# Optimization experiments

Hardware: AMD Instinct MI355X
Metric: run time of the kernel (lower is better)

## Reference

```python
import jax, jax.numpy as jnp
import numpy as np

OUT, IN = 4096, 4096      # weight_shape
VDIM = 8                  # codebook vector_dim
CODEBOOK_SIZE = 256
LEVEL = 2                 # haar_decomposition_level
INV_SQRT2 = 0.7071067811865476


def unpack_bool(packed, shape):
    # packed: int array of bytes (values 0..255); unpack 8 bits per byte (LSB first)
    bits = (packed[:, None] >> jnp.arange(8, dtype=packed.dtype)) & 1  # [n_bytes, 8]
    return bits.reshape(shape)


def inverse_haar(c, level):
    # c: [..., n] orthonormal Haar coefficients laid out [a_L, d_L, d_{L-1}, ..., d_1]
    n = c.shape[-1]
    m = n >> level
    a = c[..., :m]
    while m < n:
        d = c[..., m:2 * m]
        even = (a + d) * INV_SQRT2
        odd = (a - d) * INV_SQRT2
        a = jnp.stack([even, odd], axis=-1).reshape(c.shape[:-1] + (2 * m,))
        m *= 2
    return a


def setup_inputs() -> dict:
    key = jax.random.key(0)
    k1, k2, k3, k4, k5 = jax.random.split(key, 5)
    x = jax.random.normal(k1, (4, 2048, IN), dtype=jnp.float32)
    codebook = jax.random.normal(k2, (CODEBOOK_SIZE, VDIM), dtype=jnp.float32)
    scales = jax.random.uniform(k5, (OUT, 1), dtype=jnp.float32)
    indices = jax.random.randint(k3, (OUT * IN // VDIM,), 0, CODEBOOK_SIZE, dtype=jnp.int32)
    signs_packed = jax.random.randint(k4, (OUT * IN // 8,), 0, 256, dtype=jnp.int32)
    return {"x": x, "codebook": codebook, "scales": scales,
            "indices": indices, "signs_packed": signs_packed}


def reference(x, codebook, scales, indices, signs_packed):
    # codebook gather -> haar-domain magnitudes, reshaped to signs_shape = weight shape
    haar_freq = codebook[indices].reshape(OUT, IN)
    # unpack sign bits and map {0,1} -> {-1,+1}
    signs = 2.0 * unpack_bool(signs_packed, (OUT, IN)).astype(haar_freq.dtype) - 1.0
    haar_freq = haar_freq * signs
    # multi-level inverse Haar wavelet along in_features
    w = inverse_haar(haar_freq, LEVEL)
    w = w * scales  # per-output-row scales
    return jnp.einsum('bsi,oi->bso', x, w)
```

## Files before the change

### kernel.cpp

```cpp
#include <hip/hip_runtime.h>
#include <hip/hip_bf16.h>

typedef unsigned short u16;
typedef unsigned int u32;
typedef float f32x4 __attribute__((ext_vector_type(4)));
typedef u16 u16x4 __attribute__((ext_vector_type(4)));
typedef u16 u16x8 __attribute__((ext_vector_type(8)));
typedef __bf16 bf16x8 __attribute__((ext_vector_type(8)));

#define OUT_DIM 4096
#define IN_DIM  4096
#define M_DIM   8192

__device__ __forceinline__ u16 f2bf(float f) {
  u32 u = __builtin_bit_cast(u32, f);
  return (u16)((u + 0x7FFFu + ((u >> 16) & 1u)) >> 16);
}

__global__ __launch_bounds__(256) void build_w_kernel(
    const float* __restrict__ codebook, const float* __restrict__ scales,
    const int* __restrict__ indices, const int* __restrict__ signs,
    u16* __restrict__ W) {
  __shared__ float c[IN_DIM];
  const int o   = blockIdx.x;
  const int tid = threadIdx.x;
  for (int g = tid; g < IN_DIM / 8; g += 256) {
    const int idx = indices[o * (IN_DIM / 8) + g];
    const int sp  = signs[o * (IN_DIM / 8) + g];
    f32x4 c0 = *(const f32x4*)&codebook[idx * 8];
    f32x4 c1 = *(const f32x4*)&codebook[idx * 8 + 4];
    float v[8] = {c0[0], c0[1], c0[2], c0[3], c1[0], c1[1], c1[2], c1[3]};
#pragma unroll
    for (int j = 0; j < 8; ++j)
      c[g * 8 + j] = ((sp >> j) & 1) ? v[j] : -v[j];
  }
  __syncthreads();
  const float scale = scales[o];
  const float S = 0.70710678118654752440f;
  for (int t = tid; t < IN_DIM / 4; t += 256) {
    float a   = c[t];
    float d1  = c[IN_DIM / 4 + t];
    float d2a = c[IN_DIM / 2 + 2 * t];
    float d2b = c[IN_DIM / 2 + 2 * t + 1];
    float e  = (a + d1) * S;
    float od = (a - d1) * S;
    u16x4 w;
    w[0] = f2bf((e  + d2a) * S * scale);
    w[1] = f2bf((e  - d2a) * S * scale);
    w[2] = f2bf((od + d2b) * S * scale);
    w[3] = f2bf((od - d2b) * S * scale);
    *(u16x4*)&W[(size_t)o * IN_DIM + 4 * t] = w;
  }
}

__global__ __launch_bounds__(256) void cvt_x_kernel(
    const float* __restrict__ X, u16* __restrict__ Xb) {
  const int stride = gridDim.x * blockDim.x;
  const int n8 = (M_DIM * IN_DIM) / 8;
  for (int i = blockIdx.x * blockDim.x + threadIdx.x; i < n8; i += stride) {
    f32x4 a = *(const f32x4*)&X[(size_t)i * 8];
    f32x4 b = *(const f32x4*)&X[(size_t)i * 8 + 4];
    u16x8 r;
    r[0] = f2bf(a[0]); r[1] = f2bf(a[1]); r[2] = f2bf(a[2]); r[3] = f2bf(a[3]);
    r[4] = f2bf(b[0]); r[5] = f2bf(b[1]); r[6] = f2bf(b[2]); r[7] = f2bf(b[3]);
    *(u16x8*)&Xb[(size_t)i * 8] = r;
  }
}

__global__ __launch_bounds__(512, 1) void gemm_bt_kernel(
    const u16* __restrict__ A,
    const u16* __restrict__ B,
    float*     __restrict__ C) {
  constexpr int K   = IN_DIM;
  constexpr int NT  = K / 64;
  constexpr int NIT = NT / 2;
  extern __shared__ char smem[];

  const int tid  = threadIdx.x;
  const int wave = tid >> 6;
  const int lane = tid & 63;

  const int swz = (blockIdx.x & 7) * 64 + (blockIdx.x >> 3);
  const int bm = (swz >> 4) * 256;
  const int bn = (swz & 15) * 256;

  const int wr  = (wave >> 2) * 128;
  const int wc  = (wave & 3) * 64;
  const int fr  = lane & 15;
  const int fkB = (lane >> 4) * 16;

  int offA[2][4], offB[4];
#pragma unroll
  for (int mq = 0; mq < 2; ++mq)
#pragma unroll
    for (int m = 0; m < 4; ++m) {
      int o = (wr + mq * 64 + m * 16 + fr) * 64 + fkB;
      offA[mq][m] = o ^ ((o >> 3) & 0x30);
    }
#pragma unroll
  for (int n = 0; n < 4; ++n) {
    int o = (wc + n * 16 + fr) * 64 + fkB;
    offB[n] = 16384 + (o ^ ((o >> 3) & 0x30));
  }

  const int d0 = tid * 16,        d1 = 8192 + tid * 16;
  const int l0 = d0 ^ ((d0 >> 3) & 0x30), l1 = d1 ^ ((d1 >> 3) & 0x30);
  const u16* srcA0 = A + (size_t)(bm + (d0 >> 6)) * K + ((l0 & 63) >> 1);
  const u16* srcA1 = A + (size_t)(bm + (d1 >> 6)) * K + ((l1 & 63) >> 1);
  const u16* srcB0 = B + (size_t)(bn + (d0 >> 6)) * K + ((l0 & 63) >> 1);
  const u16* srcB1 = B + (size_t)(bn + (d1 >> 6)) * K + ((l1 & 63) >> 1);
  const int ldsW = wave * 1024;

#define GLD(SRC, DST)                                              \
  __builtin_amdgcn_global_load_lds(                                \
      (const __attribute__((address_space(1))) void*)(SRC),        \
      (__attribute__((address_space(3))) void*)(DST), 16, 0, 0)

  auto stageRegion = [&](int bufi, int ks, int tile) {
    char* base = smem + bufi * 65536 + ks * 32768 + ldsW;
    const u16* a0 = srcA0 + tile * 64 + ks * 32;
    const u16* a1 = srcA1 + tile * 64 + ks * 32;
    const u16* b0 = srcB0 + tile * 64 + ks * 32;
    const u16* b1 = srcB1 + tile * 64 + ks * 32;
    GLD(a0, base);
    GLD(a1, base + 8192);
    GLD(b0, base + 16384);
    GLD(b1, base + 24576);
  };

  f32x4 acc[8][4] = {};
  bf16x8 aq[4], bq[4];

  stageRegion(0, 0, 0);
  stageRegion(0, 1, 0);
  stageRegion(1, 0, 1);
  asm volatile("s_waitcnt vmcnt(8)" ::: "memory");
  __builtin_amdgcn_s_barrier();

#define PHASE(BUFI, KS, MQ, READB, STAGE, GATE)                              \
  {                                                                          \
    const char* rb = smem + (BUFI) * 65536 + (KS) * 32768;                   \
    if (READB) {                                                             \
      _Pragma("unroll")                                                      \
      for (int n = 0; n < 4; ++n) bq[n] = *(const bf16x8*)(rb + offB[n]);    \
    }                                                                        \
    _Pragma("unroll")                                                        \
    for (int m = 0; m < 4; ++m) aq[m] = *(const bf16x8*)(rb + offA[MQ][m]);  \
    STAGE;                                                                   \
    GATE;                                                                    \
    __builtin_amdgcn_s_barrier();                                            \
    asm volatile("s_waitcnt lgkmcnt(0)" ::: "memory");                       \
    __builtin_amdgcn_s_setprio(1);                                           \
    _Pragma("unroll")                                                        \
    for (int m = 0; m < 4; ++m)                                              \
      _Pragma("unroll")                                                      \
      for (int n = 0; n < 4; ++n)                                            \
        acc[(MQ) * 4 + m][n] = __builtin_amdgcn_mfma_f32_16x16x32_bf16(      \
            aq[m], bq[n], acc[(MQ) * 4 + m][n], 0, 0, 0);                    \
    __builtin_amdgcn_s_setprio(0);                                           \
  }

#define VM8 asm volatile("s_waitcnt vmcnt(8)" ::: "memory")
#define VM4 asm volatile("s_waitcnt vmcnt(4)" ::: "memory")
#define VM0 asm volatile("s_waitcnt vmcnt(0)" ::: "memory")

  for (int i = 0; i < NIT - 1; ++i) {
    const int t0 = 2 * i;
    PHASE(0, 0, 0, 1, , )
    PHASE(0, 0, 1, 0, stageRegion(1, 1, t0 + 1), VM8)
    PHASE(0, 1, 0, 1, , )
    PHASE(0, 1, 1, 0, stageRegion(0, 0, t0 + 2), VM8)
    PHASE(1, 0, 0, 1, , )
    PHASE(1, 0, 1, 0, stageRegion(0, 1, t0 + 2), VM8)
    PHASE(1, 1, 0, 1, , )
    PHASE(1, 1, 1, 0, stageRegion(1, 0, t0 + 3), VM8)
  }

  PHASE(0, 0, 0, 1, , )
  PHASE(0, 0, 1, 0, stageRegion(1, 1, NT - 1), VM8)
  PHASE(0, 1, 0, 1, , )
  PHASE(0, 1, 1, 0, , VM4)
  PHASE(1, 0, 0, 1, , )
  PHASE(1, 0, 1, 0, , VM0)
  PHASE(1, 1, 0, 1, , )
  PHASE(1, 1, 1, 0, , )
#undef PHASE
#undef GLD
#undef VM8
#undef VM4
#undef VM0

#pragma unroll
  for (int h = 0; h < 8; ++h)
#pragma unroll
    for (int n = 0; n < 4; ++n) {
      const int col = bn + wc + n * 16 + fr;
#pragma unroll
      for (int j = 0; j < 4; ++j) {
        const int row = bm + wr + h * 16 + (lane >> 4) * 4 + j;
        C[(size_t)row * OUT_DIM + col] = acc[h][n][j];
      }
    }
}

extern "C" void kernel_launch(void* const* d_in, const int* in_sizes, int n_in,
                              void* d_out, int out_size, void* d_ws, size_t ws_size,
                              hipStream_t stream) {
  const float* x        = (const float*)d_in[0];
  const float* codebook = (const float*)d_in[1];
  const float* scales   = (const float*)d_in[2];
  const int*   indices  = (const int*)d_in[3];
  const int*   signs    = (const int*)d_in[4];
  float* out = (float*)d_out;

  u16* W  = (u16*)d_ws;
  u16* Xb = (u16*)d_ws + (size_t)OUT_DIM * IN_DIM;

  (void)hipFuncSetAttribute((const void*)gemm_bt_kernel,
                            hipFuncAttributeMaxDynamicSharedMemorySize, 131072);

  build_w_kernel<<<OUT_DIM, 256, 0, stream>>>(codebook, scales, indices, signs, W);
  cvt_x_kernel<<<2048, 256, 0, stream>>>(x, Xb);
  gemm_bt_kernel<<<(M_DIM / 256) * (OUT_DIM / 256), 512, 131072, stream>>>(Xb, W, out);
}
```

Baseline: 277.4 us.

## Restructure GEMM main loop into paired phases with one barrier per k-slice

The GEMM inner loop now handles both 64-row A halves of each k-slice in one PAIR block. It uses a single workgroup barrier per slice instead of two. The second A-half LDS reads are issued after the first batch of MFMAs, so they overlap compute instead of sitting behind a barrier and an explicit lgkmcnt(0). The global-to-LDS prefetch schedule is reworked to stage one region ahead with vmcnt(4) gates. This shortens the prefetch distance from the earlier three-region lead, which risks exposing more global load latency in exchange for less synchronisation.

```diff
diff --git a/kernel.cpp b/kernel.cpp
--- a/kernel.cpp
+++ b/kernel.cpp
@@ -73,7 +73,7 @@
     float*     __restrict__ C) {
   constexpr int K   = IN_DIM;
   constexpr int NT  = K / 64;
-  constexpr int NIT = NT / 2;
+  constexpr int NJ  = NT / 2;
   extern __shared__ char smem[];
 
   const int tid  = threadIdx.x;
@@ -129,66 +129,64 @@
   };
 
   f32x4 acc[8][4] = {};
-  bf16x8 aq[4], bq[4];
-
-  stageRegion(0, 0, 0);
-  stageRegion(0, 1, 0);
-  stageRegion(1, 0, 1);
-  asm volatile("s_waitcnt vmcnt(8)" ::: "memory");
-  __builtin_amdgcn_s_barrier();
-
-#define PHASE(BUFI, KS, MQ, READB, STAGE, GATE)                              \
+  bf16x8 aqA[4], aqB[4], bq[4];
+
+#define VM4 asm volatile("s_waitcnt vmcnt(4)" ::: "memory")
+#define VM0 asm volatile("s_waitcnt vmcnt(0)" ::: "memory")
+#define BARM asm volatile("s_barrier" ::: "memory")
+
+#define PAIR(BUFI, KS, STG, GATE)                                            \
   {                                                                          \
     const char* rb = smem + (BUFI) * 65536 + (KS) * 32768;                   \
-    if (READB) {                                                             \
-      _Pragma("unroll")                                                      \
-      for (int n = 0; n < 4; ++n) bq[n] = *(const bf16x8*)(rb + offB[n]);    \
-    }                                                                        \
-    _Pragma("unroll")                                                        \
-    for (int m = 0; m < 4; ++m) aq[m] = *(const bf16x8*)(rb + offA[MQ][m]);  \
-    STAGE;                                                                   \
+    _Pragma("unroll")                                                        \
+    for (int n = 0; n < 4; ++n) bq[n] = *(const bf16x8*)(rb + offB[n]);      \
+    _Pragma("unroll")                                                        \
+    for (int m = 0; m < 4; ++m) aqA[m] = *(const bf16x8*)(rb + offA[0][m]);  \
+    STG;                                                                     \
     GATE;                                                                    \
-    __builtin_amdgcn_s_barrier();                                            \
-    asm volatile("s_waitcnt lgkmcnt(0)" ::: "memory");                       \
+    BARM;                                                                    \
     __builtin_amdgcn_s_setprio(1);                                           \
     _Pragma("unroll")                                                        \
     for (int m = 0; m < 4; ++m)                                              \
       _Pragma("unroll")                                                      \
       for (int n = 0; n < 4; ++n)                                            \
-        acc[(MQ) * 4 + m][n] = __builtin_amdgcn_mfma_f32_16x16x32_bf16(      \
-            aq[m], bq[n], acc[(MQ) * 4 + m][n], 0, 0, 0);                    \
+        acc[m][n] = __builtin_amdgcn_mfma_f32_16x16x32_bf16(                 \
+            aqA[m], bq[n], acc[m][n], 0, 0, 0);                              \
     __builtin_amdgcn_s_setprio(0);                                           \
-  }
-
-#define VM8 asm volatile("s_waitcnt vmcnt(8)" ::: "memory")
-#define VM4 asm volatile("s_waitcnt vmcnt(4)" ::: "memory")
-#define VM0 asm volatile("s_waitcnt vmcnt(0)" ::: "memory")
-
-  for (int i = 0; i < NIT - 1; ++i) {
-    const int t0 = 2 * i;
-    PHASE(0, 0, 0, 1, , )
-    PHASE(0, 0, 1, 0, stageRegion(1, 1, t0 + 1), VM8)
-    PHASE(0, 1, 0, 1, , )
-    PHASE(0, 1, 1, 0, stageRegion(0, 0, t0 + 2), VM8)
-    PHASE(1, 0, 0, 1, , )
-    PHASE(1, 0, 1, 0, stageRegion(0, 1, t0 + 2), VM8)
-    PHASE(1, 1, 0, 1, , )
-    PHASE(1, 1, 1, 0, stageRegion(1, 0, t0 + 3), VM8)
-  }
-
-  PHASE(0, 0, 0, 1, , )
-  PHASE(0, 0, 1, 0, stageRegion(1, 1, NT - 1), VM8)
-  PHASE(0, 1, 0, 1, , )
-  PHASE(0, 1, 1, 0, , VM4)
-  PHASE(1, 0, 0, 1, , )
-  PHASE(1, 0, 1, 0, , VM0)
-  PHASE(1, 1, 0, 1, , )
-  PHASE(1, 1, 1, 0, , )
-#undef PHASE
+    _Pragma("unroll")                                                        \
+    for (int m = 0; m < 4; ++m) aqB[m] = *(const bf16x8*)(rb + offA[1][m]);  \
+    __builtin_amdgcn_s_setprio(1);                                           \
+    _Pragma("unroll")                                                        \
+    for (int m = 0; m < 4; ++m)                                              \
+      _Pragma("unroll")                                                      \
+      for (int n = 0; n < 4; ++n)                                            \
+        acc[4 + m][n] = __builtin_amdgcn_mfma_f32_16x16x32_bf16(             \
+            aqB[m], bq[n], acc[4 + m][n], 0, 0, 0);                          \
+    __builtin_amdgcn_s_setprio(0);                                           \
+  }
+
+  stageRegion(0, 0, 0);
+  stageRegion(0, 1, 0);
+  VM4;
+  BARM;
+
+  for (int j = 0; j < NJ - 1; ++j) {
+    const int t0 = 2 * j;
+    PAIR(0, 0, stageRegion(1, 0, t0 + 1), VM4)
+    PAIR(0, 1, stageRegion(1, 1, t0 + 1), VM4)
+    PAIR(1, 0, stageRegion(0, 0, t0 + 2), VM4)
+    PAIR(1, 1, stageRegion(0, 1, t0 + 2), VM4)
+  }
+
+  PAIR(0, 0, stageRegion(1, 0, NT - 1), VM4)
+  PAIR(0, 1, stageRegion(1, 1, NT - 1), VM4)
+  PAIR(1, 0, , VM0)
+  PAIR(1, 1, , )
+#undef PAIR
 #undef GLD
-#undef VM8
 #undef VM4
 #undef VM0
+#undef BARM
 
 #pragma unroll
   for (int h = 0; h < 8; ++h)
```

Result: no change. 278.9 us (+0.5%).
